# Performance work log

Measured on AMD Instinct MI355X. Metric: run time of the kernel, lower is better.

The kernel has to match this reference:

```python
import jax, jax.numpy as jnp
import numpy as np
import math

B, H, W, C = 8, 32, 32, 512
NUM_HEAD_CHANNELS = 64
NUM_HEADS = C // NUM_HEAD_CHANNELS  # 8
HEAD_DIM = C // NUM_HEADS            # 64
NUM_GROUPS = max(1, C // 16)         # 32
EPS = 1e-6  # flax GroupNorm default epsilon


def setup_inputs() -> dict:
    key = jax.random.key(0)
    ks = jax.random.split(key, 7)
    s = lambda fan: 1.0 / math.sqrt(fan)
    return {
        "x": jax.random.normal(ks[0], (B, H, W, C), jnp.float32),
        "gn_scale": jnp.ones((C,), jnp.float32),
        "gn_bias": jnp.zeros((C,), jnp.float32),
        "w_qkv": jax.random.normal(ks[1], (C, 3 * C), jnp.float32) * s(C),
        "b_qkv": jnp.zeros((3 * C,), jnp.float32),
        "w_out": jax.random.normal(ks[2], (C, C), jnp.float32) * s(C),
        "b_out": jnp.zeros((C,), jnp.float32),
    }


def _group_norm(x, scale, bias):
    # x: (B,H,W,C); normalize per (batch, group) over spatial + in-group channels
    b, h, w, c = x.shape
    xg = x.reshape(b, h * w, NUM_GROUPS, c // NUM_GROUPS)
    mu = jnp.mean(xg, axis=(1, 3), keepdims=True)
    var = jnp.var(xg, axis=(1, 3), keepdims=True)
    xn = (xg - mu) * jax.lax.rsqrt(var + EPS)
    return xn.reshape(b, h, w, c) * scale + bias


def reference(x, gn_scale, gn_bias, w_qkv, b_qkv, w_out, b_out):
    b, h, w, c = x.shape
    seq = h * w
    x_flat = x.reshape(b, seq, c)
    x_norm = _group_norm(x, gn_scale, gn_bias).reshape(b, seq, c)
    qkv = x_norm @ w_qkv + b_qkv                      # (b, seq, 3c)
    q, k, v = jnp.split(qkv, 3, axis=-1)
    scale = 1.0 / math.sqrt(HEAD_DIM)

    def to_heads(t):
        return t.reshape(b, seq, NUM_HEADS, HEAD_DIM).transpose(0, 2, 1, 3)

    q, k, v = to_heads(q), to_heads(k), to_heads(v)
    # NOTE: scale applied to both q and k, matching the original module
    weight = jnp.einsum('bhld,bhsd->bhls', q * scale, k * scale)
    weight = jax.nn.softmax(weight, axis=-1)
    out = jnp.einsum('bhls,bhsd->bhld', weight, v)
    out = out.transpose(0, 2, 1, 3).reshape(b, seq, c)
    out = out @ w_out + b_out
    return (x_flat + out).reshape(b, h, w, c)
```

## Files before the change

### kernel.cpp

```cpp
#include <hip/hip_runtime.h>
#include <hip/hip_bf16.h>

#define SEQ   1024
#define CH    512
#define NHEAD 8
#define HDIM  64
#define BATCH 8

using short8  = __attribute__((ext_vector_type(8))) short;
using short4v = __attribute__((ext_vector_type(4))) short;
using floatx4 = __attribute__((ext_vector_type(4))) float;
using uint4v  = __attribute__((ext_vector_type(4))) unsigned int;

#if __has_builtin(__builtin_amdgcn_exp2f)
#define EXP2F __builtin_amdgcn_exp2f
#else
#define EXP2F exp2f
#endif

__device__ inline unsigned short f2bf(float f) {
  __hip_bfloat16 h = __float2bfloat16(f);
  return __builtin_bit_cast(unsigned short, h);
}

__device__ inline unsigned int cvt_pk_bf16(float lo, float hi) {
  unsigned int r;
  asm("v_cvt_pk_bf16_f32 %0, %1, %2" : "=v"(r) : "v"(lo), "v"(hi));
  return r;
}

__device__ inline void load_lds16(const void* g, void* l) {
  __builtin_amdgcn_global_load_lds(
      (const __attribute__((address_space(1))) unsigned int*)g,
      (__attribute__((address_space(3))) unsigned int*)l, 16, 0, 0);
}

__global__ __launch_bounds__(1024) void prep_kernel(
    const float* __restrict__ wqkv, const float* __restrict__ wout,
    const float* __restrict__ x, const float* __restrict__ gsc,
    const float* __restrict__ gbs,
    unsigned short* __restrict__ wqkvt, unsigned short* __restrict__ woutt,
    unsigned short* __restrict__ xn) {
  __shared__ float SH[16416];
  const int blk = blockIdx.x, tid = threadIdx.x;

  if (blk >= 256) {
    const float* src; unsigned short* dst; int C, bx, by;
    if (blk < 448) { int t = blk - 256; src = wqkv; dst = wqkvt; C = 1536; bx = t % 24; by = t / 24; }
    else           { int t = blk - 448; src = wout; dst = woutt; C = 512;  bx = t & 7;  by = t >> 3; }
    float (*T)[65] = (float(*)[65])SH;
    int tx = tid & 63, ty = tid >> 6;
    for (int j = 0; j < 4; ++j)
      T[ty + j * 16][tx] = src[(size_t)(by * 64 + ty + j * 16) * C + bx * 64 + tx];
    __syncthreads();
    for (int j = 0; j < 4; ++j)
      dst[(size_t)(bx * 64 + ty + j * 16) * 512 + by * 64 + tx] = f2bf(T[tx][ty + j * 16]);
    return;
  }

  const int b = blk >> 5, g = blk & 31;
  const size_t base = (size_t)b * SEQ * CH + g * 16;

  float s = 0.f, sq = 0.f;
  for (int i = 0; i < 4; ++i) {
    int c = (i << 10) + tid;
    int r = c >> 2, c4 = (c & 3) << 2;
    float4 v = *(const float4*)(x + base + (size_t)r * CH + c4);
    *(float4*)&SH[c << 2] = v;
    s  += v.x + v.y + v.z + v.w;
    sq += v.x * v.x + v.y * v.y + v.z * v.z + v.w * v.w;
  }
  for (int off = 1; off < 64; off <<= 1) {
    s  += __shfl_xor(s, off);
    sq += __shfl_xor(sq, off);
  }
  const int wid = tid >> 6, lane = tid & 63;
  if (lane == 0) { SH[16384 + wid] = s; SH[16400 + wid] = sq; }
  __syncthreads();
  float ts = 0.f, tq = 0.f;
  for (int i = 0; i < 16; ++i) { ts += SH[16384 + i]; tq += SH[16400 + i]; }
  const float inv_n = 1.0f / 16384.0f;
  float mean = ts * inv_n;
  float var  = tq * inv_n - mean * mean;
  float rstd = rsqrtf(var + 1e-6f);

  int c4 = (tid & 3) << 2;
  float4 sc = *(const float4*)(gsc + g * 16 + c4);
  float4 bs = *(const float4*)(gbs + g * 16 + c4);
  for (int i = 0; i < 4; ++i) {
    int c = (i << 10) + tid;
    int r = c >> 2;
    float4 v = *(const float4*)&SH[c << 2];
    ushort4 o;
    o.x = f2bf((v.x - mean) * rstd * sc.x + bs.x);
    o.y = f2bf((v.y - mean) * rstd * sc.y + bs.y);
    o.z = f2bf((v.z - mean) * rstd * sc.z + bs.z);
    o.w = f2bf((v.w - mean) * rstd * sc.w + bs.w);
    *(ushort4*)(xn + base + (size_t)r * CH + c4) = o;
  }
}

template <int EPI, int MTILE>
__global__ __launch_bounds__(256) void gemm_bt_kernel(
    const unsigned short* __restrict__ A, const unsigned short* __restrict__ Bt,
    int K, int N,
    const float* __restrict__ bias, const float* __restrict__ resid,
    float* __restrict__ outf,
    unsigned short* __restrict__ qb, unsigned short* __restrict__ kb,
    unsigned short* __restrict__ vtb) {
  constexpr int SMSZ = (MTILE == 128) ? 17408 : 16896;
  constexpr int NI   = (MTILE == 128) ? 4 : 2;
  __shared__ alignas(16) unsigned short SM[SMSZ];
  unsigned short* LA = SM;
  unsigned short* LB = SM + MTILE * 64;

  const int tid = threadIdx.x;
  const int wid = tid >> 6, lane = tid & 63;
  const int quad = lane >> 4, m16 = lane & 15;
  const int sw = m16 & 7;
  const int wm = (MTILE == 128) ? (wid & 1) * 64 : 0;
  const int wn = (MTILE == 128) ? (wid >> 1) * 64 : wid * 32;
  const int m0 = blockIdx.x * MTILE, n0 = blockIdx.y * 128;

  floatx4 acc[4][NI];
  for (int i = 0; i < 4; ++i)
    for (int j = 0; j < NI; ++j) acc[i][j] = 0.f;

  for (int k0 = 0; k0 < K; k0 += 64) {
    for (int i = 0; i < MTILE / 32; ++i) {
      int c = i * 256 + tid;
      int r = c >> 3, kc = c & 7;
      load_lds16(A + (size_t)(m0 + r) * K + k0 + ((kc ^ (r & 7)) << 3), &LA[c << 3]);
    }
    for (int i = 0; i < 4; ++i) {
      int c = i * 256 + tid;
      int r = c >> 3, kc = c & 7;
      load_lds16(Bt + (size_t)(n0 + r) * K + k0 + ((kc ^ (r & 7)) << 3), &LB[c << 3]);
    }
    __syncthreads();
    for (int kq = 0; kq < 2; ++kq) {
      int csw = (((kq << 2) + quad) ^ sw) << 3;
      short8 af[4], bf[NI];
      for (int mi = 0; mi < 4; ++mi)
        af[mi] = *(const short8*)&LA[(wm + mi * 16 + m16) * 64 + csw];
      for (int ni = 0; ni < NI; ++ni)
        bf[ni] = *(const short8*)&LB[(wn + ni * 16 + m16) * 64 + csw];
      for (int mi = 0; mi < 4; ++mi)
        for (int ni = 0; ni < NI; ++ni)
          acc[mi][ni] = __builtin_amdgcn_mfma_f32_16x16x32_bf16(af[mi], bf[ni], acc[mi][ni], 0, 0, 0);
    }
    __syncthreads();
  }

  const int b = m0 >> 10;
  if (EPI == 0) {
    const int part = n0 >> 9;
    if (part < 2) {
      const float qscale = (part == 0) ? 0.0225421381f : 1.0f;
      unsigned short* dst = (part == 0) ? qb : kb;
      for (int mi = 0; mi < 4; ++mi)
        for (int ni = 0; ni < 4; ++ni) {
          int ln = wn + ni * 16 + m16;
          float bb = bias[n0 + ln];
          for (int reg = 0; reg < 4; ++reg)
            SM[(wm + mi * 16 + quad * 4 + reg) * 136 + ln] =
                f2bf((acc[mi][ni][reg] + bb) * qscale);
        }
      __syncthreads();
      const int colb = n0 & 511;
      for (int j = 0; j < 8; ++j) {
        int c = j * 256 + tid;
        int m = c >> 4, n8 = (c & 15) * 8;
        int h = (colb + n8) >> 6, d = n8 & 63;
        int sp = (m0 & 1023) + m;
        int4 v = *(const int4*)&SM[m * 136 + n8];
        *(int4*)(dst + (((size_t)(b * NHEAD + h)) * SEQ + sp) * HDIM + d) = v;
      }
    } else {
      for (int mi = 0; mi < 4; ++mi)
        for (int ni = 0; ni < 4; ++ni) {
          int ln = wn + ni * 16 + m16;
          float bb = bias[n0 + ln];
          int mblk = (wm >> 4) + mi;
          int sbase = 32 * (mblk >> 1) + 8 * quad + 4 * (mblk & 1);
          for (int reg = 0; reg < 4; ++reg)
            SM[ln * 136 + sbase + reg] = f2bf(acc[mi][ni][reg] + bb);
        }
      __syncthreads();
      int hbase = (n0 - 1024) >> 6;
      for (int j = 0; j < 8; ++j) {
        int c = j * 256 + tid;
        int ld = c >> 4, sp8 = (c & 15) * 8;
        int h = hbase + (ld >> 6), d = ld & 63;
        int4 v = *(const int4*)&SM[ld * 136 + sp8];
        *(int4*)(vtb + ((size_t)(b * NHEAD + h) * HDIM + d) * SEQ + (m0 & 1023) + sp8) = v;
      }
    }
  } else {
    float* SMf = (float*)SM;
    for (int mi = 0; mi < 4; ++mi)
      for (int ni = 0; ni < NI; ++ni) {
        int ln = wn + ni * 16 + m16;
        float bb = bias[n0 + ln];
        for (int reg = 0; reg < 4; ++reg)
          SMf[(mi * 16 + quad * 4 + reg) * 132 + ln] = acc[mi][ni][reg] + bb;
      }
    __syncthreads();
    for (int j = 0; j < 8; ++j) {
      int c = j * 256 + tid;
      int m = c >> 5, n4 = (c & 31) * 4;
      size_t idx = (size_t)(m0 + m) * N + n0 + n4;
      float4 v = *(const float4*)&SMf[m * 132 + n4];
      float4 rr = *(const float4*)&resid[idx];
      v.x += rr.x; v.y += rr.y; v.z += rr.z; v.w += rr.w;
      *(float4*)&outf[idx] = v;
    }
  }
}

__global__ __launch_bounds__(512) void attn_kernel(
    const unsigned short* __restrict__ qb, const unsigned short* __restrict__ kb,
    const unsigned short* __restrict__ vtb, unsigned short* __restrict__ ao) {
  const int head = blockIdx.x, qt = blockIdx.y;
  const int b = head >> 3, h = head & 7;
  const int tid = threadIdx.x;
  const int wid = tid >> 6, lane = tid & 63;
  const int quad = lane >> 4, m16 = lane & 15;
  const int sw = m16 & 7;

  __shared__ alignas(16) unsigned short sK[2][8192];
  __shared__ alignas(16) unsigned short sV[2][8192];

  const unsigned short* kbase = kb  + (size_t)head * SEQ * HDIM;
  const unsigned short* vbase = vtb + (size_t)head * HDIM * SEQ;

  const size_t qrow = (size_t)head * SEQ + qt * 128 + wid * 16 + m16;
  short8 aq0 = *(const short8*)(qb + qrow * HDIM + quad * 8);
  short8 aq1 = *(const short8*)(qb + qrow * HDIM + 32 + quad * 8);

  const unsigned int onep = 0x3F803F80u;
  const short8 vones = __builtin_bit_cast(short8, (uint4v){onep, onep, onep, onep});

  floatx4 la = 0.f;
  floatx4 o[4];
  for (int df = 0; df < 4; ++df) o[df] = 0.f;

  for (int i = 0; i < 2; ++i) {
    int c = i * 512 + tid;
    int r = c >> 3, kc = c & 7;
    load_lds16(kbase + r * HDIM + ((kc ^ (r & 7)) << 3), &sK[0][c << 3]);
  }
  for (int i = 0; i < 2; ++i) {
    int c = i * 512 + tid;
    int d = c >> 4, kc = c & 15;
    load_lds16(vbase + d * SEQ + ((kc ^ (d & 7)) << 3), &sV[0][c << 3]);
  }
  __syncthreads();

  int buf = 0;
  for (int kt = 0; kt < 8; ++kt) {
    if (kt < 7) {
      const int nb = buf ^ 1, kn = kt + 1;
      for (int i = 0; i < 2; ++i) {
        int c = i * 512 + tid;
        int r = c >> 3, kc = c & 7;
        load_lds16(kbase + (kn * 128 + r) * HDIM + ((kc ^ (r & 7)) << 3), &sK[nb][c << 3]);
      }
      for (int i = 0; i < 2; ++i) {
        int c = i * 512 + tid;
        int d = c >> 4, kc = c & 15;
        load_lds16(vbase + d * SEQ + kn * 128 + ((kc ^ (d & 7)) << 3), &sV[nb][c << 3]);
      }
    }

    unsigned int pw[4][4];
    for (int sf = 0; sf < 8; ++sf) {
      const int rb = (sf * 16 + m16) * 64;
      short8 k0 = *(const short8*)&sK[buf][rb + ((quad ^ sw) << 3)];
      short8 k1 = *(const short8*)&sK[buf][rb + (((4 + quad) ^ sw) << 3)];
      floatx4 s = 0.f;
      __builtin_amdgcn_s_setprio(1);
      s = __builtin_amdgcn_mfma_f32_16x16x32_bf16(k0, aq0, s, 0, 0, 0);
      s = __builtin_amdgcn_mfma_f32_16x16x32_bf16(k1, aq1, s, 0, 0, 0);
      __builtin_amdgcn_s_setprio(0);
      float p0 = EXP2F(s[0]), p1 = EXP2F(s[1]);
      float p2 = EXP2F(s[2]), p3 = EXP2F(s[3]);
      const int u = sf >> 1, w2 = (sf & 1) * 2;
      pw[u][w2 + 0] = cvt_pk_bf16(p0, p1);
      pw[u][w2 + 1] = cvt_pk_bf16(p2, p3);
    }

    for (int u = 0; u < 4; ++u) {
      const short8 pf = __builtin_bit_cast(
          short8, (uint4v){pw[u][0], pw[u][1], pw[u][2], pw[u][3]});
      const int chunk = ((u * 4 + quad) ^ sw) << 3;
      __builtin_amdgcn_s_setprio(1);
      for (int df = 0; df < 4; ++df) {
        short8 bv = *(const short8*)&sV[buf][(df * 16 + m16) * 128 + chunk];
        o[df] = __builtin_amdgcn_mfma_f32_16x16x32_bf16(pf, bv, o[df], 0, 0, 0);
      }
      la = __builtin_amdgcn_mfma_f32_16x16x32_bf16(pf, vones, la, 0, 0, 0);
      __builtin_amdgcn_s_setprio(0);
    }
    __syncthreads();
    buf ^= 1;
  }

  floatx4 lr;
  for (int r = 0; r < 4; ++r) lr[r] = 1.0f / la[r];
  int qg = qt * 128 + wid * 16 + quad * 4;
  for (int df = 0; df < 4; ++df) {
    int col = h * HDIM + df * 16 + m16;
    size_t base = (size_t)(b * SEQ + qg) * CH + col;
    ao[base + 0 * CH] = f2bf(o[df][0] * lr[0]);
    ao[base + 1 * CH] = f2bf(o[df][1] * lr[1]);
    ao[base + 2 * CH] = f2bf(o[df][2] * lr[2]);
    ao[base + 3 * CH] = f2bf(o[df][3] * lr[3]);
  }
}

extern "C" void kernel_launch(void* const* d_in, const int* in_sizes, int n_in,
                              void* d_out, int out_size, void* d_ws, size_t ws_size,
                              hipStream_t stream) {
  const float* x    = (const float*)d_in[0];
  const float* gsc  = (const float*)d_in[1];
  const float* gbs  = (const float*)d_in[2];
  const float* wqkv = (const float*)d_in[3];
  const float* bqkv = (const float*)d_in[4];
  const float* wout = (const float*)d_in[5];
  const float* bout = (const float*)d_in[6];
  float* out = (float*)d_out;

  char* ws = (char*)d_ws;
  unsigned short* xn    = (unsigned short*)(ws);
  unsigned short* wqkvt = (unsigned short*)(ws + 8388608);
  unsigned short* woutt = (unsigned short*)(ws + 9961472);
  unsigned short* qb    = (unsigned short*)(ws + 10485760);
  unsigned short* kb    = (unsigned short*)(ws + 18874368);
  unsigned short* vtb   = (unsigned short*)(ws + 27262976);
  unsigned short* ao    = (unsigned short*)(ws + 35651584);

  prep_kernel<<<512, 1024, 0, stream>>>(wqkv, wout, x, gsc, gbs, wqkvt, woutt, xn);
  gemm_bt_kernel<0, 128><<<dim3(64, 12), 256, 0, stream>>>(
      xn, wqkvt, 512, 1536, bqkv, nullptr, nullptr, qb, kb, vtb);
  attn_kernel<<<dim3(64, 8), 512, 0, stream>>>(qb, kb, vtb, ao);
  gemm_bt_kernel<1, 64><<<dim3(128, 4), 256, 0, stream>>>(
      ao, woutt, 512, 512, bout, x, out, nullptr, nullptr, nullptr);
}
```

Before: 144.9 us.

## Process two query blocks per wave in attention to reuse K/V fragments

The attention kernel now runs 4 waves (256 threads) per block instead of 8. Each wave handles 32 query rows (two 16-row blocks) instead of 16, and each K and V fragment read from LDS feeds two MFMAs. This halves LDS reads per unit of work. The cost is doubled accumulator and P registers per wave and fewer waves per block to hide latency, so occupancy may drop.

```diff
diff --git a/kernel.cpp b/kernel.cpp
--- a/kernel.cpp
+++ b/kernel.cpp
@@ -218,7 +218,7 @@
   }
 }
 
-__global__ __launch_bounds__(512) void attn_kernel(
+__global__ __launch_bounds__(256) void attn_kernel(
     const unsigned short* __restrict__ qb, const unsigned short* __restrict__ kb,
     const unsigned short* __restrict__ vtb, unsigned short* __restrict__ ao) {
   const int head = blockIdx.x, qt = blockIdx.y;
@@ -234,24 +234,30 @@
   const unsigned short* kbase = kb  + (size_t)head * SEQ * HDIM;
   const unsigned short* vbase = vtb + (size_t)head * HDIM * SEQ;
 
-  const size_t qrow = (size_t)head * SEQ + qt * 128 + wid * 16 + m16;
-  short8 aq0 = *(const short8*)(qb + qrow * HDIM + quad * 8);
-  short8 aq1 = *(const short8*)(qb + qrow * HDIM + 32 + quad * 8);
+  short8 aq[2][2];
+  for (int qblk = 0; qblk < 2; ++qblk) {
+    const size_t qrow = (size_t)head * SEQ + qt * 128 + wid * 32 + qblk * 16 + m16;
+    aq[qblk][0] = *(const short8*)(qb + qrow * HDIM + quad * 8);
+    aq[qblk][1] = *(const short8*)(qb + qrow * HDIM + 32 + quad * 8);
+  }
 
   const unsigned int onep = 0x3F803F80u;
   const short8 vones = __builtin_bit_cast(short8, (uint4v){onep, onep, onep, onep});
 
-  floatx4 la = 0.f;
-  floatx4 o[4];
-  for (int df = 0; df < 4; ++df) o[df] = 0.f;
-
-  for (int i = 0; i < 2; ++i) {
-    int c = i * 512 + tid;
+  floatx4 la[2];
+  floatx4 o[2][4];
+  for (int qblk = 0; qblk < 2; ++qblk) {
+    la[qblk] = 0.f;
+    for (int df = 0; df < 4; ++df) o[qblk][df] = 0.f;
+  }
+
+  for (int i = 0; i < 4; ++i) {
+    int c = i * 256 + tid;
     int r = c >> 3, kc = c & 7;
     load_lds16(kbase + r * HDIM + ((kc ^ (r & 7)) << 3), &sK[0][c << 3]);
   }
-  for (int i = 0; i < 2; ++i) {
-    int c = i * 512 + tid;
+  for (int i = 0; i < 4; ++i) {
+    int c = i * 256 + tid;
     int d = c >> 4, kc = c & 15;
     load_lds16(vbase + d * SEQ + ((kc ^ (d & 7)) << 3), &sV[0][c << 3]);
   }
@@ -261,61 +267,77 @@
   for (int kt = 0; kt < 8; ++kt) {
     if (kt < 7) {
       const int nb = buf ^ 1, kn = kt + 1;
-      for (int i = 0; i < 2; ++i) {
-        int c = i * 512 + tid;
+      for (int i = 0; i < 4; ++i) {
+        int c = i * 256 + tid;
         int r = c >> 3, kc = c & 7;
         load_lds16(kbase + (kn * 128 + r) * HDIM + ((kc ^ (r & 7)) << 3), &sK[nb][c << 3]);
       }
-      for (int i = 0; i < 2; ++i) {
-        int c = i * 512 + tid;
+      for (int i = 0; i < 4; ++i) {
+        int c = i * 256 + tid;
         int d = c >> 4, kc = c & 15;
         load_lds16(vbase + d * SEQ + kn * 128 + ((kc ^ (d & 7)) << 3), &sV[nb][c << 3]);
       }
     }
 
-    unsigned int pw[4][4];
+    unsigned int pw[2][4][4];
     for (int sf = 0; sf < 8; ++sf) {
       const int rb = (sf * 16 + m16) * 64;
       short8 k0 = *(const short8*)&sK[buf][rb + ((quad ^ sw) << 3)];
       short8 k1 = *(const short8*)&sK[buf][rb + (((4 + quad) ^ sw) << 3)];
-      floatx4 s = 0.f;
+      floatx4 s0 = 0.f, s1 = 0.f;
       __builtin_amdgcn_s_setprio(1);
-      s = __builtin_amdgcn_mfma_f32_16x16x32_bf16(k0, aq0, s, 0, 0, 0);
-      s = __builtin_amdgcn_mfma_f32_16x16x32_bf16(k1, aq1, s, 0, 0, 0);
+      s0 = __builtin_amdgcn_mfma_f32_16x16x32_bf16(k0, aq[0][0], s0, 0, 0, 0);
+      s0 = __builtin_amdgcn_mfma_f32_16x16x32_bf16(k1, aq[0][1], s0, 0, 0, 0);
+      s1 = __builtin_amdgcn_mfma_f32_16x16x32_bf16(k0, aq[1][0], s1, 0, 0, 0);
+      s1 = __builtin_amdgcn_mfma_f32_16x16x32_bf16(k1, aq[1][1], s1, 0, 0, 0);
       __builtin_amdgcn_s_setprio(0);
-      float p0 = EXP2F(s[0]), p1 = EXP2F(s[1]);
-      float p2 = EXP2F(s[2]), p3 = EXP2F(s[3]);
       const int u = sf >> 1, w2 = (sf & 1) * 2;
-      pw[u][w2 + 0] = cvt_pk_bf16(p0, p1);
-      pw[u][w2 + 1] = cvt_pk_bf16(p2, p3);
+      {
+        float p0 = EXP2F(s0[0]), p1 = EXP2F(s0[1]);
+        float p2 = EXP2F(s0[2]), p3 = EXP2F(s0[3]);
+        pw[0][u][w2 + 0] = cvt_pk_bf16(p0, p1);
+        pw[0][u][w2 + 1] = cvt_pk_bf16(p2, p3);
+      }
+      {
+        float p0 = EXP2F(s1[0]), p1 = EXP2F(s1[1]);
+        float p2 = EXP2F(s1[2]), p3 = EXP2F(s1[3]);
+        pw[1][u][w2 + 0] = cvt_pk_bf16(p0, p1);
+        pw[1][u][w2 + 1] = cvt_pk_bf16(p2, p3);
+      }
     }
 
     for (int u = 0; u < 4; ++u) {
-      const short8 pf = __builtin_bit_cast(
-          short8, (uint4v){pw[u][0], pw[u][1], pw[u][2], pw[u][3]});
+      const short8 pf0 = __builtin_bit_cast(
+          short8, (uint4v){pw[0][u][0], pw[0][u][1], pw[0][u][2], pw[0][u][3]});
+      const short8 pf1 = __builtin_bit_cast(
+          short8, (uint4v){pw[1][u][0], pw[1][u][1], pw[1][u][2], pw[1][u][3]});
       const int chunk = ((u * 4 + quad) ^ sw) << 3;
       __builtin_amdgcn_s_setprio(1);
       for (int df = 0; df < 4; ++df) {
         short8 bv = *(const short8*)&sV[buf][(df * 16 + m16) * 128 + chunk];
-        o[df] = __builtin_amdgcn_mfma_f32_16x16x32_bf16(pf, bv, o[df], 0, 0, 0);
-      }
-      la = __builtin_amdgcn_mfma_f32_16x16x32_bf16(pf, vones, la, 0, 0, 0);
+        o[0][df] = __builtin_amdgcn_mfma_f32_16x16x32_bf16(pf0, bv, o[0][df], 0, 0, 0);
+        o[1][df] = __builtin_amdgcn_mfma_f32_16x16x32_bf16(pf1, bv, o[1][df], 0, 0, 0);
+      }
+      la[0] = __builtin_amdgcn_mfma_f32_16x16x32_bf16(pf0, vones, la[0], 0, 0, 0);
+      la[1] = __builtin_amdgcn_mfma_f32_16x16x32_bf16(pf1, vones, la[1], 0, 0, 0);
       __builtin_amdgcn_s_setprio(0);
     }
     __syncthreads();
     buf ^= 1;
   }
 
-  floatx4 lr;
-  for (int r = 0; r < 4; ++r) lr[r] = 1.0f / la[r];
-  int qg = qt * 128 + wid * 16 + quad * 4;
-  for (int df = 0; df < 4; ++df) {
-    int col = h * HDIM + df * 16 + m16;
-    size_t base = (size_t)(b * SEQ + qg) * CH + col;
-    ao[base + 0 * CH] = f2bf(o[df][0] * lr[0]);
-    ao[base + 1 * CH] = f2bf(o[df][1] * lr[1]);
-    ao[base + 2 * CH] = f2bf(o[df][2] * lr[2]);
-    ao[base + 3 * CH] = f2bf(o[df][3] * lr[3]);
+  for (int qblk = 0; qblk < 2; ++qblk) {
+    floatx4 lr;
+    for (int r = 0; r < 4; ++r) lr[r] = 1.0f / la[qblk][r];
+    int qg = qt * 128 + wid * 32 + qblk * 16 + quad * 4;
+    for (int df = 0; df < 4; ++df) {
+      int col = h * HDIM + df * 16 + m16;
+      size_t base = (size_t)(b * SEQ + qg) * CH + col;
+      ao[base + 0 * CH] = f2bf(o[qblk][df][0] * lr[0]);
+      ao[base + 1 * CH] = f2bf(o[qblk][df][1] * lr[1]);
+      ao[base + 2 * CH] = f2bf(o[qblk][df][2] * lr[2]);
+      ao[base + 3 * CH] = f2bf(o[qblk][df][3] * lr[3]);
+    }
   }
 }
 
@@ -343,7 +365,7 @@
   prep_kernel<<<512, 1024, 0, stream>>>(wqkv, wout, x, gsc, gbs, wqkvt, woutt, xn);
   gemm_bt_kernel<0, 128><<<dim3(64, 12), 256, 0, stream>>>(
       xn, wqkvt, 512, 1536, bqkv, nullptr, nullptr, qb, kb, vtb);
-  attn_kernel<<<dim3(64, 8), 512, 0, stream>>>(qb, kb, vtb, ao);
+  attn_kernel<<<dim3(64, 8), 256, 0, stream>>>(qb, kb, vtb, ao);
   gemm_bt_kernel<1, 64><<<dim3(128, 4), 256, 0, stream>>>(
       ao, woutt, 512, 512, bout, x, out, nullptr, nullptr, nullptr);
 }
```

Result: no change. 145.4 us (+0.4%).
